# Performance work log

Hardware: AMD Instinct MI355X
Metric: run time of the kernel (lower is better)

The kernel has to match this reference:

```python
import jax, jax.numpy as jnp
import numpy as np

S, B, I, H, NQ = 256, 64, 512, 1024, 4


def setup_inputs() -> dict:
    key = jax.random.key(0)
    ks = jax.random.split(key, 12)
    w = lambda k, sh: jax.random.normal(k, sh, jnp.float32) * 0.05
    return {
        "inputs": jax.random.normal(ks[0], (S, B, I), jnp.float32),
        "Wf": w(ks[1], (I + H, H)), "bf": jnp.zeros((H,), jnp.float32),
        "Wi": w(ks[2], (I + H, H)), "bi": jnp.zeros((H,), jnp.float32),
        "Wu": w(ks[3], (I + H, H)), "bu": jnp.zeros((H,), jnp.float32),
        "Wo": w(ks[4], (I + H, H)), "bo": jnp.zeros((H,), jnp.float32),
        "pf": jax.random.normal(ks[5], (NQ,), jnp.float32),
        "pi_q": jax.random.normal(ks[6], (NQ,), jnp.float32),
        "pu": jax.random.normal(ks[7], (NQ,), jnp.float32),
        "po": jax.random.normal(ks[8], (NQ,), jnp.float32),
        "Wc": w(ks[9], (H + 1, H)), "bc": jnp.zeros((H,), jnp.float32),
    }


def reference(inputs, Wf, bf, Wi, bi, Wu, bu, Wo, bo, pf, pi_q, pu, po, Wc, bc):
    # inputs: (S, B, I); states initialized to zeros
    def qgate(pre, p):
        # pre: (B, H); use first NQ features -> simulated <Z> = cos(2*theta)
        theta = pre[:, :NQ] @ p  # (B,)
        return jnp.cos(2.0 * theta)[:, None]  # (B, 1)

    def comb(v):
        return v @ Wc + bc

    def step(carry, x):
        hx, cx = carry
        c = jnp.concatenate([x, hx], axis=1)  # (B, I+H)
        pre_f = c @ Wf + bf
        pre_i = c @ Wi + bi
        pre_u = c @ Wu + bu
        pre_o = c @ Wo + bo
        f = jax.nn.sigmoid(comb(jnp.concatenate(
            [jax.nn.sigmoid(pre_f), jax.nn.sigmoid(qgate(pre_f, pf))], axis=1)))
        i = jax.nn.sigmoid(comb(jnp.concatenate(
            [jax.nn.sigmoid(pre_i), jax.nn.sigmoid(qgate(pre_i, pi_q))], axis=1)))
        g = jnp.tanh(comb(jnp.concatenate(
            [jnp.tanh(pre_u), qgate(pre_u, pu)], axis=1)))  # update gate: no sigmoid on quantum part
        o = jax.nn.sigmoid(comb(jnp.concatenate(
            [jax.nn.sigmoid(pre_o), jax.nn.sigmoid(qgate(pre_o, po))], axis=1)))
        cx_new = f * cx + i * g
        hx_new = o * jnp.tanh(cx_new)
        return (hx_new, cx_new), hx_new

    init = (jnp.zeros((B, H), inputs.dtype), jnp.zeros((B, H), inputs.dtype))
    (hx, cx), outputs = jax.lax.scan(step, init, inputs)
    return outputs, (hx, cx)
```

## Files before the change

kernel.cpp:

```cpp
#include <hip/hip_runtime.h>

#define S_LEN 256
#define B_SZ 64
#define I_SZ 512
#define H_SZ 1024
#define NBLK 256

typedef __bf16 bf16x8 __attribute__((ext_vector_type(8)));
typedef float f32x4 __attribute__((ext_vector_type(4)));
typedef unsigned long long u64;

__device__ __forceinline__ float sigmoidf_(float x){ return 1.f/(1.f + expf(-x)); }

__device__ __forceinline__ u64 ld_cc64(const u64* p){
  return __hip_atomic_load(p, __ATOMIC_RELAXED, __HIP_MEMORY_SCOPE_AGENT);
}
__device__ __forceinline__ void st_cc16(__bf16* p, __bf16 v){
  unsigned short b = __builtin_bit_cast(unsigned short, v);
  __hip_atomic_store((unsigned short*)p, b, __ATOMIC_RELAXED, __HIP_MEMORY_SCOPE_AGENT);
}
__device__ __forceinline__ void st_cc32(float* p, float v){
  __hip_atomic_store(p, v, __ATOMIC_RELAXED, __HIP_MEMORY_SCOPE_AGENT);
}
__device__ __forceinline__ float ld_cc32f(const float* p){
  return __hip_atomic_load(p, __ATOMIC_RELAXED, __HIP_MEMORY_SCOPE_AGENT);
}


__global__ __launch_bounds__(64) void pack_w4_k(const float* __restrict__ Wf, const float* __restrict__ Wi,
                                                const float* __restrict__ Wu, const float* __restrict__ Wo,
                                                __bf16* __restrict__ W4p){
  int blk = blockIdx.x;
  int nt = blk / 48, kb = blk % 48;
  int l = threadIdx.x;
  int n = nt*16 + (l & 15);
  int g = n >> 10, h = n & 1023;
  const float* W = (g==0)?Wf:((g==1)?Wi:((g==2)?Wu:Wo));
  int k0 = kb*32 + ((l>>4)<<3);
  __bf16 tmp[8];
#pragma unroll
  for (int j=0;j<8;j++) tmp[j] = (__bf16)W[(size_t)(k0+j)*H_SZ + h];
  *reinterpret_cast<bf16x8*>(W4p + ((size_t)blk*64 + l)*8) = *reinterpret_cast<bf16x8*>(tmp);
}

__global__ __launch_bounds__(64) void pack_wc_k(const float* __restrict__ Wc, __bf16* __restrict__ Wcp){
  int blk = blockIdx.x;
  int nt = blk / 32, kb = blk % 32;
  int l = threadIdx.x;
  int n = nt*16 + (l & 15);
  int k0 = kb*32 + ((l>>4)<<3);
  __bf16 tmp[8];
#pragma unroll
  for (int j=0;j<8;j++) tmp[j] = (__bf16)Wc[(size_t)(k0+j)*H_SZ + n];
  *reinterpret_cast<bf16x8*>(Wcp + ((size_t)blk*64 + l)*8) = *reinterpret_cast<bf16x8*>(tmp);
}

__global__ __launch_bounds__(256) void pack_x_k(const float* __restrict__ x, __bf16* __restrict__ xF){
  int bid = blockIdx.x;
  int s = bid >> 2, mt = bid & 3;
#pragma unroll
  for (int j=0;j<4;j++){
    int G = j*256 + threadIdx.x;
    int kb = G >> 6, lane = G & 63;
    int b = mt*16 + (lane & 15);
    int k0 = kb*32 + ((lane>>4)<<3);
    const float* src = x + ((size_t)s*B_SZ + b)*I_SZ + k0;
    float4 v0 = *reinterpret_cast<const float4*>(src);
    float4 v1 = *reinterpret_cast<const float4*>(src+4);
    __bf16 t[8] = {(__bf16)v0.x,(__bf16)v0.y,(__bf16)v0.z,(__bf16)v0.w,
                   (__bf16)v1.x,(__bf16)v1.y,(__bf16)v1.z,(__bf16)v1.w};
    *reinterpret_cast<bf16x8*>(xF + ((size_t)bid*1024 + G)*8) = *reinterpret_cast<bf16x8*>(t);
  }
}

__global__ void init_h_k(__bf16* __restrict__ hxF){
  int i = blockIdx.x*blockDim.x + threadIdx.x;
  hxF[i] = (__bf16)0.f;
}

__device__ __forceinline__ void bar_arrive(unsigned* cnt){
  asm volatile("" ::: "memory");
  __syncthreads();
  if (threadIdx.x == 0)
    __hip_atomic_fetch_add(cnt, 1u, __ATOMIC_RELAXED, __HIP_MEMORY_SCOPE_AGENT);
}
__device__ __forceinline__ void bar_wait(const unsigned* cnt, unsigned target){
  if (threadIdx.x == 0){
    while (__hip_atomic_load(cnt, __ATOMIC_RELAXED, __HIP_MEMORY_SCOPE_AGENT) < target)
      __builtin_amdgcn_s_sleep(1);
  }
  __syncthreads();
}


__global__ __launch_bounds__(256, 1) void qlstm_persist_k(
    const __bf16* __restrict__ xF,
    __bf16* hxF,
    const __bf16* __restrict__ W4p, const __bf16* __restrict__ Wcp,
    const float* __restrict__ bfv, const float* __restrict__ biv,
    const float* __restrict__ buv, const float* __restrict__ bov,
    const float* __restrict__ pf, const float* __restrict__ piq,
    const float* __restrict__ pu, const float* __restrict__ po,
    const float* __restrict__ WcLast, const float* __restrict__ bc,
    __bf16* actF, float* zact,
    float* __restrict__ out,
    unsigned* bar_cnt)
{
  __shared__ __align__(16) __bf16 ldsWc[2*32*64*8];
  __shared__ __align__(16) char ldsA[32768];
  __shared__ float gx[4][8][32];
  __shared__ float pre4[16][4];

  const int tid = threadIdx.x;
  const int bid = blockIdx.x;
  const int wave = tid >> 6;
  const int l = tid & 63;
  const int col = l & 15;
  const int kq = l >> 4;

  const int mt1 = bid >> 6;
  const int nt64 = bid & 63;
  const int nt16 = nt64*4 + wave;
  const int g1 = nt16 >> 6;
  const int h1 = (nt16*16 + col) & 1023;

  const int mt2 = bid >> 5;
  const int ht  = bid & 31;
  const int r2 = tid >> 5;
  const int c2 = tid & 31;
  const int b2 = mt2*8 + r2;
  const int h2 = ht*32 + c2;
  const int slot2 = kq*8 + (l & 7);

  bf16x8 wfrag[48];
  {
    const bf16x8* src = (const bf16x8*)(W4p + ((size_t)nt16*48*64 + (size_t)l)*8);
#pragma unroll
    for (int kb=0;kb<48;kb++) wfrag[kb] = src[(size_t)kb*64];
  }
  {
    const u64* src = (const u64*)(Wcp + (size_t)(ht*2)*32*64*8);
    u64* dst = (u64*)ldsWc;
    for (int i = tid; i < 8192; i += 256) dst[i] = src[i];
  }

  const float* bptr = (g1==0)?bfv:((g1==1)?biv:((g1==2)?buv:bov));
  const float bias1 = bptr[h1];
  const bool isU1 = (g1==2);
  const bool isQb = ((nt64 & 15) == 0);
  const int gq = nt64 >> 4;
  float pq0=0.f,pq1=0.f,pq2=0.f,pq3=0.f;
  if (isQb && wave==0){
    const float* pq = (gq==0)?pf:((gq==1)?piq:((gq==2)?pu:po));
    pq0=pq[0]; pq1=pq[1]; pq2=pq[2]; pq3=pq[3];
  }

  const float wl2 = WcLast[h2];
  const float bc2 = bc[h2];
  float creg = 0.f;

  size_t eis[4];
#pragma unroll
  for (int rr=0;rr<4;rr++){
    int brow = mt1*16 + (kq<<2) + rr;
    eis[rr] = (((size_t)(g1*8 + (brow>>3))*32 + (h1>>5))*32
               + (size_t)((((h1>>3)&3)<<3) + (brow&7)))*8 + (h1&7);
  }
  const int laneh = (b2 & 15) + (((c2 >> 3) & 3) << 4);
  const size_t hei = ((size_t)((b2>>4)*32 + ht)*64 + laneh)*8 + (c2 & 7);

  __syncthreads();

  const size_t SBH = (size_t)S_LEN*B_SZ*H_SZ;

  for (int s = 0; s < S_LEN; ++s){
    {
      f32x4 acc[4] = {{0,0,0,0},{0,0,0,0},{0,0,0,0},{0,0,0,0}};
      const bf16x8* xp = (const bf16x8*)xF + (size_t)(s*4 + mt1)*1024 + l;
      {
        bf16x8 xf[8];
#pragma unroll
        for (int j=0;j<8;j++) xf[j] = xp[(size_t)j*64];
#pragma unroll
        for (int j=0;j<8;j++)
          acc[j&3] = __builtin_amdgcn_mfma_f32_16x16x32_bf16(xf[j], wfrag[j], acc[j&3], 0,0,0);
#pragma unroll
        for (int j=0;j<8;j++) xf[j] = xp[(size_t)(8+j)*64];
#pragma unroll
        for (int j=0;j<8;j++)
          acc[j&3] = __builtin_amdgcn_mfma_f32_16x16x32_bf16(xf[j], wfrag[8+j], acc[j&3], 0,0,0);
      }

      bar_wait(bar_cnt, (unsigned)(2*s)*NBLK);

      {
        const u64* hp = (const u64*)hxF + (size_t)mt1*4096;
        u64 slo[8], shi[8];
#pragma unroll
        for (int i=0;i<8;i++){
          int G = tid + 256*i;
          slo[i] = ld_cc64(hp + (size_t)G*2);
          shi[i] = ld_cc64(hp + (size_t)G*2 + 1);
        }
#pragma unroll
        for (int i=0;i<8;i++){
          int G = tid + 256*i;
          ulonglong2 v; v.x = slo[i]; v.y = shi[i];
          *reinterpret_cast<ulonglong2*>(ldsA + (size_t)G*16) = v;
        }
      }
      __syncthreads();

#pragma unroll
      for (int kb=0;kb<32;kb++){
        bf16x8 a = *reinterpret_cast<const bf16x8*>(ldsA + ((size_t)kb*64 + l)*16);
        acc[kb&3] = __builtin_amdgcn_mfma_f32_16x16x32_bf16(a, wfrag[16+kb], acc[kb&3], 0,0,0);
      }
      f32x4 r = (acc[0]+acc[1])+(acc[2]+acc[3]);
      float pr[4];
#pragma unroll
      for (int rr=0;rr<4;rr++){
        float p = r[rr] + bias1;
        pr[rr] = p;
        float a = isU1 ? tanhf(p) : sigmoidf_(p);
        st_cc16(&actF[eis[rr]], (__bf16)a);
      }
      if (isQb && wave==0){
        if (col < 4){
#pragma unroll
          for (int rr=0;rr<4;rr++) pre4[(kq<<2)+rr][col] = pr[rr];
        }
        if (l < 16){
          float th = pre4[l][0]*pq0 + pre4[l][1]*pq1 + pre4[l][2]*pq2 + pre4[l][3]*pq3;
          float z = cosf(2.f*th);
          st_cc32(&zact[gq*B_SZ + mt1*16 + l], (gq==2) ? z : sigmoidf_(z));
        }
      }
    }

    bar_arrive(bar_cnt);
    bar_wait(bar_cnt, (unsigned)(2*s+1)*NBLK);

    {
      float zf = ld_cc32f(&zact[      b2]);
      float zi = ld_cc32f(&zact[ 64 + b2]);
      float zu = ld_cc32f(&zact[128 + b2]);
      float zo = ld_cc32f(&zact[192 + b2]);

      const u64* ap = (const u64*)actF + (size_t)(wave*8 + mt2)*2048 + (size_t)slot2*2;
      const bf16x8* bf0 = (const bf16x8*)ldsWc + l;
      const bf16x8* bf1 = bf0 + 2048;
      f32x4 acc2[4] = {{0,0,0,0},{0,0,0,0},{0,0,0,0},{0,0,0,0}};
      u64 A0lo[8], A0hi[8], A1lo[8], A1hi[8];
#pragma unroll
      for (int i=0;i<8;i++){
        A0lo[i] = ld_cc64(ap + (size_t)i*64);
        A0hi[i] = ld_cc64(ap + (size_t)i*64 + 1);
      }
#pragma unroll
      for (int c=0;c<4;c++){
        u64* clo = (c&1) ? A1lo : A0lo;
        u64* chi = (c&1) ? A1hi : A0hi;
        u64* nlo = (c&1) ? A0lo : A1lo;
        u64* nhi = (c&1) ? A0hi : A1hi;
        if (c < 3){
#pragma unroll
          for (int i=0;i<8;i++){
            nlo[i] = ld_cc64(ap + (size_t)((c+1)*8 + i)*64);
            nhi[i] = ld_cc64(ap + (size_t)((c+1)*8 + i)*64 + 1);
          }
        }
#pragma unroll
        for (int i=0;i<8;i++){
          int kb = c*8 + i;
          union{u64 u[2]; bf16x8 v;} a; a.u[0]=clo[i]; a.u[1]=chi[i];
          acc2[kb&1]     = __builtin_amdgcn_mfma_f32_16x16x32_bf16(a.v, bf0[(size_t)kb*64], acc2[kb&1], 0,0,0);
          acc2[2+(kb&1)] = __builtin_amdgcn_mfma_f32_16x16x32_bf16(a.v, bf1[(size_t)kb*64], acc2[2+(kb&1)], 0,0,0);
        }
      }
      f32x4 rA = acc2[0]+acc2[1];
      f32x4 rB = acc2[2]+acc2[3];
#pragma unroll
      for (int rr=0;rr<4;rr++){
        int row = (kq<<2) + rr;
        if (row < 8){
          gx[wave][row][col]      = rA[rr];
          gx[wave][row][16 + col] = rB[rr];
        }
      }
      __syncthreads();

      float fg = sigmoidf_(gx[0][r2][c2] + bc2 + zf*wl2);
      float ig = sigmoidf_(gx[1][r2][c2] + bc2 + zi*wl2);
      float gg = tanhf(    gx[2][r2][c2] + bc2 + zu*wl2);
      float og = sigmoidf_(gx[3][r2][c2] + bc2 + zo*wl2);
      float cn = fg*creg + ig*gg;
      creg = cn;
      float hn = og*tanhf(cn);
      st_cc16(&hxF[hei], (__bf16)hn);
      size_t idx = (size_t)b2*H_SZ + h2;
      __builtin_nontemporal_store(hn, &out[(size_t)s*B_SZ*H_SZ + idx]);
      if (s == S_LEN-1){
        __builtin_nontemporal_store(hn, &out[SBH + idx]);
        __builtin_nontemporal_store(cn, &out[SBH + (size_t)B_SZ*H_SZ + idx]);
      }
    }

    bar_arrive(bar_cnt);
  }
}


extern "C" void kernel_launch(void* const* d_in, const int* in_sizes, int n_in,
                              void* d_out, int out_size, void* d_ws, size_t ws_size,
                              hipStream_t stream){
  const float* inputs = (const float*)d_in[0];
  const float* Wf  = (const float*)d_in[1];
  const float* bf_ = (const float*)d_in[2];
  const float* Wi  = (const float*)d_in[3];
  const float* bi_ = (const float*)d_in[4];
  const float* Wu  = (const float*)d_in[5];
  const float* bu_ = (const float*)d_in[6];
  const float* Wo  = (const float*)d_in[7];
  const float* bo_ = (const float*)d_in[8];
  const float* pf  = (const float*)d_in[9];
  const float* piq = (const float*)d_in[10];
  const float* pu  = (const float*)d_in[11];
  const float* po  = (const float*)d_in[12];
  const float* Wc  = (const float*)d_in[13];
  const float* bc  = (const float*)d_in[14];
  float* out = (float*)d_out;

  __bf16* W4p = (__bf16*)d_ws;
  __bf16* Wcp = W4p + (size_t)256*48*64*8;
  __bf16* xF  = Wcp + (size_t)64*32*64*8;
  __bf16* actF = xF + (size_t)S_LEN*B_SZ*I_SZ;
  __bf16* hxF = actF + (size_t)4*B_SZ*H_SZ;
  float*  zact = (float*)(hxF + (size_t)B_SZ*H_SZ);
  unsigned* bar = (unsigned*)(zact + 256);

  pack_w4_k<<<256*48, 64, 0, stream>>>(Wf, Wi, Wu, Wo, W4p);
  pack_wc_k<<<64*32, 64, 0, stream>>>(Wc, Wcp);
  pack_x_k<<<S_LEN*4, 256, 0, stream>>>(inputs, xF);
  init_h_k<<<256, 256, 0, stream>>>(hxF);
  hipMemsetAsync(bar, 0, 256*sizeof(unsigned), stream);

  qlstm_persist_k<<<NBLK, 256, 0, stream>>>(
      xF, hxF, W4p, Wcp, bf_, bi_, bu_, bo_, pf, piq, pu, po,
      Wc + (size_t)H_SZ*H_SZ, bc, actF, zact, out, bar);
}
```

Measured before the change: 3.396 ms.

## Replace global atomic barrier with per-group flag barriers over 64 blocks

```diff
diff --git a/kernel.cpp b/kernel.cpp
--- a/kernel.cpp
+++ b/kernel.cpp
@@ -78,16 +78,22 @@
   hxF[i] = (__bf16)0.f;
 }
 
-__device__ __forceinline__ void bar_arrive(unsigned* cnt){
+__device__ __forceinline__ void bar_arrive(unsigned* flags, int gbase, int sub, unsigned target){
   asm volatile("" ::: "memory");
   __syncthreads();
-  if (threadIdx.x == 0)
-    __hip_atomic_fetch_add(cnt, 1u, __ATOMIC_RELAXED, __HIP_MEMORY_SCOPE_AGENT);
-}
-__device__ __forceinline__ void bar_wait(const unsigned* cnt, unsigned target){
   if (threadIdx.x == 0){
-    while (__hip_atomic_load(cnt, __ATOMIC_RELAXED, __HIP_MEMORY_SCOPE_AGENT) < target)
+    __builtin_amdgcn_fence(__ATOMIC_RELEASE, "agent");
+    __hip_atomic_store(&flags[gbase + sub], target, __ATOMIC_RELAXED, __HIP_MEMORY_SCOPE_AGENT);
+  }
+}
+__device__ __forceinline__ void bar_wait(const unsigned* flags, int gbase, unsigned target){
+  if (threadIdx.x < 64){
+    const unsigned* f = flags + gbase + threadIdx.x;
+    for(;;){
+      unsigned v = __hip_atomic_load(f, __ATOMIC_RELAXED, __HIP_MEMORY_SCOPE_AGENT);
+      if (__all(v >= target)) break;
       __builtin_amdgcn_s_sleep(1);
+    }
   }
   __syncthreads();
 }
@@ -104,7 +110,7 @@
     const float* __restrict__ WcLast, const float* __restrict__ bc,
     __bf16* actF, float* zact,
     float* __restrict__ out,
-    unsigned* bar_cnt)
+    unsigned* flags)
 {
   __shared__ __align__(16) __bf16 ldsWc[2*32*64*8];
   __shared__ __align__(16) char ldsA[32768];
@@ -118,8 +124,12 @@
   const int col = l & 15;
   const int kq = l >> 4;
 
-  const int mt1 = bid >> 6;
-  const int nt64 = bid & 63;
+  const int grp = bid >> 6;
+  const int sub = bid & 63;
+  const int gbase = grp * 64;
+
+  const int mt1 = grp;
+  const int nt64 = sub;
   const int nt16 = nt64*4 + wave;
   const int g1 = nt16 >> 6;
   const int h1 = (nt16*16 + col) & 1023;
@@ -191,7 +201,7 @@
           acc[j&3] = __builtin_amdgcn_mfma_f32_16x16x32_bf16(xf[j], wfrag[8+j], acc[j&3], 0,0,0);
       }
 
-      bar_wait(bar_cnt, (unsigned)(2*s)*NBLK);
+      bar_wait(flags, gbase, (unsigned)(2*s));
 
       {
         const u64* hp = (const u64*)hxF + (size_t)mt1*4096;
@@ -238,8 +248,8 @@
       }
     }
 
-    bar_arrive(bar_cnt);
-    bar_wait(bar_cnt, (unsigned)(2*s+1)*NBLK);
+    bar_arrive(flags, gbase, sub, (unsigned)(2*s+1));
+    bar_wait(flags, gbase, (unsigned)(2*s+1));
 
     {
       float zf = ld_cc32f(&zact[      b2]);
@@ -306,7 +316,7 @@
       }
     }
 
-    bar_arrive(bar_cnt);
+    bar_arrive(flags, gbase, sub, (unsigned)(2*s+2));
   }
 }
 
@@ -337,15 +347,15 @@
   __bf16* actF = xF + (size_t)S_LEN*B_SZ*I_SZ;
   __bf16* hxF = actF + (size_t)4*B_SZ*H_SZ;
   float*  zact = (float*)(hxF + (size_t)B_SZ*H_SZ);
-  unsigned* bar = (unsigned*)(zact + 256);
+  unsigned* flags = (unsigned*)(zact + 256);
 
   pack_w4_k<<<256*48, 64, 0, stream>>>(Wf, Wi, Wu, Wo, W4p);
   pack_wc_k<<<64*32, 64, 0, stream>>>(Wc, Wcp);
   pack_x_k<<<S_LEN*4, 256, 0, stream>>>(inputs, xF);
   init_h_k<<<256, 256, 0, stream>>>(hxF);
-  hipMemsetAsync(bar, 0, 256*sizeof(unsigned), stream);
+  hipMemsetAsync(flags, 0, NBLK*sizeof(unsigned), stream);
 
   qlstm_persist_k<<<NBLK, 256, 0, stream>>>(
       xF, hxF, W4p, Wcp, bf_, bi_, bu_, bo_, pf, piq, pu, po,
-      Wc + (size_t)H_SZ*H_SZ, bc, actF, zact, out, bar);
-}
+      Wc + (size_t)H_SZ*H_SZ, bc, actF, zact, out, flags);
+}
```

Result: slower. 5.148 ms (+51.6%).
